# Kernel tuning notes

Hardware: AMD Instinct MI355X
Metric: run time of the kernel (lower is better)

## Reference

```python
import jax, jax.numpy as jnp
import numpy as np

K = 20          # neighbors, hardcoded default in source
EPS = 1e-5      # BatchNorm2d default eps


def _knn(x, k=K):
    # x: (B, C, N). distance[b,i,j] = -||x_i - x_j||^2; top-k == first k of descending sort
    inner = -2.0 * jnp.einsum('bdn,bdm->bnm', x, x)
    xx = jnp.sum(x * x, axis=1)                      # (B, N)
    dist = -xx[:, :, None] - inner - xx[:, None, :]  # (B, N, N)
    return jax.lax.top_k(dist, k)[1]                 # (B, N, k) int32


def _graph_feature(x, k=K):
    idx = _knn(x, k)
    xt = jnp.transpose(x, (0, 2, 1))                 # (B, N, C)
    feat = jax.vmap(lambda a, i: a[i])(xt, idx)      # (B, N, k, C) gather
    center = jnp.broadcast_to(xt[:, :, None, :], feat.shape)
    out = jnp.concatenate([feat - center, center], axis=-1)  # (B, N, k, 2C)
    return jnp.transpose(out, (0, 3, 1, 2))          # (B, 2C, N, k)


def _conv_bn_relu(x, w, g, b):
    # 1x1 conv (no bias) + train-mode BatchNorm (batch stats) + ReLU
    y = jnp.einsum('oc,bcnk->bonk', w, x)
    m = jnp.mean(y, axis=(0, 2, 3), keepdims=True)
    v = jnp.var(y, axis=(0, 2, 3), keepdims=True)
    y = (y - m) * jax.lax.rsqrt(v + EPS)
    y = y * g[None, :, None, None] + b[None, :, None, None]
    return jax.nn.relu(y)


def setup_inputs() -> dict:
    key = jax.random.key(0)
    ks = jax.random.split(key, 8)
    B, C, N = 8, 3, 2048
    emb = 512
    x = jax.random.normal(ks[0], (B, C, N), dtype=jnp.float32)

    def w(k, o, i):
        return jax.random.normal(k, (o, i), dtype=jnp.float32) * np.sqrt(2.0 / i).astype(np.float32)

    d = {'x': x}
    dims = [(6, 64), (64, 64), (64, 128), (128, 256), (512, emb)]
    for n, (i, o) in enumerate(dims, start=1):
        d[f'w{n}'] = w(ks[n], o, i)
        d[f'g{n}'] = jnp.ones((o,), jnp.float32)
        d[f'b{n}'] = jnp.zeros((o,), jnp.float32)
    return d


def reference(x, w1, g1, b1, w2, g2, b2, w3, g3, b3, w4, g4, b4, w5, g5, b5):
    B, _, N = x.shape
    h = _graph_feature(x)                                  # (B, 6, N, k)
    h = _conv_bn_relu(h, w1, g1, b1); x1 = jnp.max(h, -1, keepdims=True)
    h = _conv_bn_relu(h, w2, g2, b2); x2 = jnp.max(h, -1, keepdims=True)
    h = _conv_bn_relu(h, w3, g3, b3); x3 = jnp.max(h, -1, keepdims=True)
    h = _conv_bn_relu(h, w4, g4, b4); x4 = jnp.max(h, -1, keepdims=True)
    o = jnp.concatenate([x1, x2, x3, x4], axis=1)          # (B, 512, N, 1)
    o = _conv_bn_relu(o, w5, g5, b5)                       # (B, 512, N, 1)
    return o.reshape(B, -1, N)
```

## Files before the change

kernel.cpp:

```cpp
#include <hip/hip_runtime.h>
#include <cstdint>
#include <cstddef>

#define BATCH 8
#define NPTS 2048
#define KNN 20
#define M1 327680
#define M2 16384

typedef unsigned short ushort_t;
typedef __attribute__((ext_vector_type(8))) short bf16x8;
typedef __attribute__((ext_vector_type(4))) float f32x4;
typedef __attribute__((ext_vector_type(2))) int int2v;

#define OFF_XT    0UL
#define OFF_XX    196608UL
#define OFF_IDX   262144UL
#define OFF_WH2   1572864UL
#define OFF_WH3   1589248UL
#define OFF_WH4   1622016UL
#define OFF_WH5   1753088UL
#define OFF_SS    2842624UL
#define OFF_REG0  2863104UL
#define OFF_REG1  86749184UL
#define OFF_XCAT  128692224UL
#define OFF_RAWMAX 145469440UL
#define OFF_RAWMIN 162246656UL
#define OFF_SP     179023872UL
#define WS_NEEDED  181121024UL

__device__ __forceinline__ float bf2f(unsigned short u) {
    union { unsigned int i; float f; } c; c.i = ((unsigned int)u) << 16; return c.f;
}
__device__ __forceinline__ unsigned short f2bf(float f) {
    union { float f; unsigned int i; } c; c.f = f;
    unsigned int x = c.i;
    unsigned int r = (x + 0x7fffu + ((x >> 16) & 1u)) >> 16;
    return (unsigned short)r;
}
__device__ __forceinline__ unsigned int pack2(float a, float b) {
    return (unsigned int)f2bf(a) | ((unsigned int)f2bf(b) << 16);
}
__device__ __forceinline__ void unpack8(uint4 u, float* v) {
    v[0] = bf2f((unsigned short)(u.x & 0xffffu)); v[1] = bf2f((unsigned short)(u.x >> 16));
    v[2] = bf2f((unsigned short)(u.y & 0xffffu)); v[3] = bf2f((unsigned short)(u.y >> 16));
    v[4] = bf2f((unsigned short)(u.z & 0xffffu)); v[5] = bf2f((unsigned short)(u.z >> 16));
    v[6] = bf2f((unsigned short)(u.w & 0xffffu)); v[7] = bf2f((unsigned short)(u.w >> 16));
}

__global__ void prep_k(const float* __restrict__ x, float* __restrict__ xt, float* __restrict__ xx) {
    int t = blockIdx.x * 256 + threadIdx.x;
    int b = t >> 11, n = t & 2047;
    float v0 = x[((size_t)b * 3 + 0) * NPTS + n];
    float v1 = x[((size_t)b * 3 + 1) * NPTS + n];
    float v2 = x[((size_t)b * 3 + 2) * NPTS + n];
    xt[(size_t)t * 3 + 0] = v0; xt[(size_t)t * 3 + 1] = v1; xt[(size_t)t * 3 + 2] = v2;
    xx[t] = __fadd_rn(__fadd_rn(__fmul_rn(v0, v0), __fmul_rn(v1, v1)), __fmul_rn(v2, v2));
}

__global__ void wsplit_all_k(const float* __restrict__ w2, ushort_t* __restrict__ wh2,
                             const float* __restrict__ w3, ushort_t* __restrict__ wh3,
                             const float* __restrict__ w4, ushort_t* __restrict__ wh4,
                             const float* __restrict__ w5, ushort_t* __restrict__ wh5) {
    int t = blockIdx.x * 256 + threadIdx.x;
    if (t < 4096)        { wh2[t] = f2bf(w2[t]); }
    else if (t < 12288)  { int o = t - 4096;  wh3[o] = f2bf(w3[o]); }
    else if (t < 45056)  { int o = t - 12288; wh4[o] = f2bf(w4[o]); }
    else                 { int o = t - 45056; wh5[o] = f2bf(w5[o]); }
}


__device__ __forceinline__ unsigned okey(float f) {
    int u = __float_as_int(f);
    return (unsigned)(u ^ ((u >> 31) | 0x80000000));
}

#define DPP_ROR(x, n) __builtin_amdgcn_update_dpp(0, (x), 0x120 + (n), 0xf, 0xf, true)

template<int N>
__device__ __forceinline__ void ror_merge(unsigned &hi, unsigned &lo) {
    unsigned thi = (unsigned)DPP_ROR((int)hi, N);
    unsigned tlo = (unsigned)DPP_ROR((int)lo, N);
    unsigned long long a = ((unsigned long long)hi << 32) | lo;
    unsigned long long b = ((unsigned long long)thi << 32) | tlo;
    if (b > a) { hi = thi; lo = tlo; }
}

__device__ __forceinline__ void half_merge(unsigned &hi, unsigned &lo) {
    int2v ph = __builtin_amdgcn_permlane32_swap((int)hi, (int)hi, false, false);
    int2v pl = __builtin_amdgcn_permlane32_swap((int)lo, (int)lo, false, false);
    unsigned long long a = ((unsigned long long)(unsigned)ph.x << 32) | (unsigned)pl.x;
    unsigned long long b = ((unsigned long long)(unsigned)ph.y << 32) | (unsigned)pl.y;
    if (b > a) { hi = (unsigned)ph.y; lo = (unsigned)pl.y; }
    else       { hi = (unsigned)ph.x; lo = (unsigned)pl.x; }
}

__device__ __forceinline__ int knn_winner(unsigned hi, unsigned lo) {
    unsigned h0 = (unsigned)__builtin_amdgcn_readlane((int)hi, 0);
    unsigned l0 = (unsigned)__builtin_amdgcn_readlane((int)lo, 0);
    unsigned h1 = (unsigned)__builtin_amdgcn_readlane((int)hi, 16);
    unsigned l1 = (unsigned)__builtin_amdgcn_readlane((int)lo, 16);
    unsigned long long A = ((unsigned long long)h0 << 32) | l0;
    unsigned long long B = ((unsigned long long)h1 << 32) | l1;
    unsigned lw = (B > A) ? l1 : l0;
    return 2047 - (int)lw;
}

template<int G>
__device__ __forceinline__ void knn_rescan(float (&v)[32], unsigned (&gh)[4], unsigned (&gl)[4],
                                           bool own, int qw, unsigned laneC) {
#pragma unroll
    for (int q = G * 8; q < G * 8 + 8; q++)
        if (own && q == qw) v[q] = -3.4e38f;
    float m = v[G * 8]; int qi = G * 8;
#pragma unroll
    for (int q = G * 8 + 1; q < G * 8 + 8; q++)
        if (v[q] > m) { m = v[q]; qi = q; }
    gh[G] = okey(m);
    gl[G] = laneC - (unsigned)(qi << 6);
}

__device__ __forceinline__ void knn_rescan_any(float (&v)[32], unsigned (&gh)[4], unsigned (&gl)[4],
                                               int j, int l, unsigned laneC) {
    int qw = j >> 6;
    bool own = (l == (j & 63));
    int gw = qw >> 3;
    if (gw == 0)      knn_rescan<0>(v, gh, gl, own, qw, laneC);
    else if (gw == 1) knn_rescan<1>(v, gh, gl, own, qw, laneC);
    else if (gw == 2) knn_rescan<2>(v, gh, gl, own, qw, laneC);
    else              knn_rescan<3>(v, gh, gl, own, qw, laneC);
}

__launch_bounds__(256)
__global__ void knn_k(const float* __restrict__ xt, const float* __restrict__ xx, int* __restrict__ idx) {
    int tid = threadIdx.x;
    int l = tid & 63, wv = tid >> 6;
    int pidA = blockIdx.x * 8 + wv * 2;
    int pidB = pidA + 1;
    int b = pidA >> 11;
    const float* xb  = xt + (size_t)b * NPTS * 3;
    const float* xxb = xx + (size_t)b * NPTS;
    int iA = pidA & 2047, iB = pidB & 2047;
    float xA0 = xb[iA * 3 + 0], xA1 = xb[iA * 3 + 1], xA2 = xb[iA * 3 + 2];
    float xB0 = xb[iB * 3 + 0], xB1 = xb[iB * 3 + 1], xB2 = xb[iB * 3 + 2];
    float xxA = xxb[iA], xxB = xxb[iB];
    float vA[32], vB[32];
#pragma unroll
    for (int q = 0; q < 32; q++) {
        int j = l + q * 64;
        float p0 = xb[j * 3 + 0], p1 = xb[j * 3 + 1], p2 = xb[j * 3 + 2];
        float xxj = xxb[j];
        float dA = __fadd_rn(__fadd_rn(__fmul_rn(xA0, p0), __fmul_rn(xA1, p1)), __fmul_rn(xA2, p2));
        float dB = __fadd_rn(__fadd_rn(__fmul_rn(xB0, p0), __fmul_rn(xB1, p1)), __fmul_rn(xB2, p2));
        vA[q] = __fsub_rn(__fsub_rn(-xxA, __fmul_rn(-2.0f, dA)), xxj);
        vB[q] = __fsub_rn(__fsub_rn(-xxB, __fmul_rn(-2.0f, dB)), xxj);
    }
    unsigned laneC = (unsigned)(2047 - l);
    unsigned ghA[4], glA[4], ghB[4], glB[4];
#pragma unroll
    for (int g = 0; g < 4; g++) {
        float mA = vA[g * 8]; int qA = g * 8;
        float mB = vB[g * 8]; int qB = g * 8;
#pragma unroll
        for (int q = g * 8 + 1; q < g * 8 + 8; q++) {
            if (vA[q] > mA) { mA = vA[q]; qA = q; }
            if (vB[q] > mB) { mB = vB[q]; qB = q; }
        }
        ghA[g] = okey(mA); glA[g] = laneC - (unsigned)(qA << 6);
        ghB[g] = okey(mB); glB[g] = laneC - (unsigned)(qB << 6);
    }
    int* outA = idx + (size_t)pidA * KNN;
    int* outB = idx + (size_t)pidB * KNN;
    for (int t = 0; t < KNN; t++) {
        unsigned hA = ghA[0], lA = glA[0];
        unsigned hB = ghB[0], lB = glB[0];
#pragma unroll
        for (int g = 1; g < 4; g++) {
            unsigned long long a0 = ((unsigned long long)hA << 32) | lA;
            unsigned long long b0 = ((unsigned long long)ghA[g] << 32) | glA[g];
            if (b0 > a0) { hA = ghA[g]; lA = glA[g]; }
            unsigned long long a1 = ((unsigned long long)hB << 32) | lB;
            unsigned long long b1 = ((unsigned long long)ghB[g] << 32) | glB[g];
            if (b1 > a1) { hB = ghB[g]; lB = glB[g]; }
        }
        ror_merge<1>(hA, lA); ror_merge<1>(hB, lB);
        ror_merge<2>(hA, lA); ror_merge<2>(hB, lB);
        ror_merge<4>(hA, lA); ror_merge<4>(hB, lB);
        ror_merge<8>(hA, lA); ror_merge<8>(hB, lB);
        half_merge(hA, lA);   half_merge(hB, lB);
        int jA = knn_winner(hA, lA);
        int jB = knn_winner(hB, lB);
        if (l == 0) { outA[t] = jA; outB[t] = jB; }
        if (t == KNN - 1) break;
        knn_rescan_any(vA, ghA, glA, jA, l, laneC);
        knn_rescan_any(vB, ghB, glB, jB, l, laneC);
    }
}

__launch_bounds__(256, 2)
__global__ void conv1_fused_k(const float* __restrict__ xt, const int* __restrict__ idx,
                              const float* __restrict__ w1, ushort_t* __restrict__ y1,
                              float* __restrict__ rawmax, float* __restrict__ rawmin,
                              float* __restrict__ sp) {
    __shared__ ushort_t hA[320 * 56];
    __shared__ ushort_t wHs[64 * 56];
    __shared__ float sw[4 * 64 * 2];
    const int tid = threadIdx.x;
    const int m0 = blockIdx.x * 320;
    for (int i = tid; i < 512; i += 256) sw[i] = 0.0f;
    {
        int row = tid >> 2, seg = tid & 3;
        uint4 u = make_uint4(0, 0, 0, 0);
        if (seg == 0) {
            const float* wr = w1 + row * 6;
            u.x = pack2(wr[0], wr[1]);
            u.y = pack2(wr[2], wr[3]);
            u.z = pack2(wr[4], wr[5]);
        }
        *(uint4*)&wHs[row * 56 + seg * 8] = u;
    }
    for (int r = tid; r < 320; r += 256) {
        int m = m0 + r;
        int nb = m / KNN;
        int b = nb >> 11;
        int j = idx[m];
        const float* pi = xt + (size_t)nb * 3;
        const float* pj = xt + ((size_t)(b * NPTS + j)) * 3;
        uint4 u;
        u.x = pack2(pj[0] - pi[0], pj[1] - pi[1]);
        u.y = pack2(pj[2] - pi[2], pi[0]);
        u.z = pack2(pi[1], pi[2]);
        u.w = 0;
        uint4 z = make_uint4(0, 0, 0, 0);
        *(uint4*)&hA[r * 56 + 0]  = u;
        *(uint4*)&hA[r * 56 + 8]  = z;
        *(uint4*)&hA[r * 56 + 16] = z;
        *(uint4*)&hA[r * 56 + 24] = z;
    }
    __syncthreads();
    const int lane = tid & 63, wv = tid >> 6;
    const int l15 = lane & 15, quad = lane >> 4;
    f32x4 acc[5][4];
#pragma unroll
    for (int mt = 0; mt < 5; mt++)
#pragma unroll
        for (int ot = 0; ot < 4; ot++) acc[mt][ot] = (f32x4){0.f, 0.f, 0.f, 0.f};
    bf16x8 a[5];
#pragma unroll
    for (int mt = 0; mt < 5; mt++)
        a[mt] = *(bf16x8*)&hA[(wv * 80 + mt * 16 + l15) * 56 + quad * 8];
#pragma unroll
    for (int ot = 0; ot < 4; ot++) {
        bf16x8 bh = *(bf16x8*)&wHs[(ot * 16 + l15) * 56 + quad * 8];
#pragma unroll
        for (int mt = 0; mt < 5; mt++)
            acc[mt][ot] = __builtin_amdgcn_mfma_f32_16x16x32_bf16(a[mt], bh, acc[mt][ot], 0, 0, 0);
    }
    __syncthreads();
    float* wreg = (float*)((char*)hA + wv * 6400);
#pragma unroll
    for (int ot = 0; ot < 4; ot++) {
#pragma unroll
        for (int mt = 0; mt < 5; mt++)
#pragma unroll
            for (int r = 0; r < 4; r++)
                wreg[(mt * 16 + quad * 4 + r) * 20 + l15] = acc[mt][ot][r];
        __syncthreads();
        {
            int pp = quad;
            const float* rr = wreg + (pp * 20) * 20 + l15;
            float mx = rr[0], mn = rr[0], sm = 0.0f, ss = 0.0f;
#pragma unroll
            for (int q = 0; q < 20; q++) {
                float vv = rr[q * 20];
                mx = fmaxf(mx, vv); mn = fminf(mn, vv);
                sm += vv; ss = fmaf(vv, vv, ss);
            }
            int pt = blockIdx.x * 16 + wv * 4 + pp;
            int o = ot * 16 + l15;
            rawmax[(size_t)pt * 64 + o] = mx;
            rawmin[(size_t)pt * 64 + o] = mn;
            sm += __shfl_xor(sm, 16); sm += __shfl_xor(sm, 32);
            ss += __shfl_xor(ss, 16); ss += __shfl_xor(ss, 32);
            if (lane < 16) {
                sw[(wv * 64 + ot * 16 + l15) * 2 + 0] += sm;
                sw[(wv * 64 + ot * 16 + l15) * 2 + 1] += ss;
            }
        }
#pragma unroll
        for (int it = 0; it < 3; it++) {
            int t = lane + it * 64;
            if (t < 160) {
                int row = t >> 1, half = t & 1;
                float4 f0 = *(float4*)&wreg[row * 20 + half * 8];
                float4 f1 = *(float4*)&wreg[row * 20 + half * 8 + 4];
                uint4 u;
                u.x = pack2(f0.x, f0.y); u.y = pack2(f0.z, f0.w);
                u.z = pack2(f1.x, f1.y); u.w = pack2(f1.z, f1.w);
                *(uint4*)(y1 + (size_t)(m0 + wv * 80 + row) * 64 + ot * 16 + half * 8) = u;
            }
        }
        __syncthreads();
    }
    if (tid < 128) {
        int ol = tid >> 1, st = tid & 1;
        float v = 0.0f;
#pragma unroll
        for (int w2 = 0; w2 < 4; w2++) v += sw[(w2 * 64 + ol) * 2 + st];
        sp[(size_t)blockIdx.x * 128 + ol * 2 + st] = v;
    }
}

template<int CIN, int COUT>
__launch_bounds__(256)
__global__ void conv5_mfma_k(const ushort_t* __restrict__ yin,
                             const ushort_t* __restrict__ whi,
                             ushort_t* __restrict__ yout,
                             float* __restrict__ sp) {
    __shared__ char smem[23552];
    ushort_t* hA = (ushort_t*)smem;
    ushort_t* wH = (ushort_t*)(smem + 14336);
    float* sw = (float*)(smem + 21504);
    const int tid = threadIdx.x;
    const int m0 = blockIdx.y * 128;
    const int o0 = blockIdx.x * 64;
    f32x4 acc[2][4];
#pragma unroll
    for (int mt = 0; mt < 2; mt++)
#pragma unroll
        for (int ot = 0; ot < 4; ot++) acc[mt][ot] = (f32x4){0.f, 0.f, 0.f, 0.f};
    const int lane = tid & 63, wv = tid >> 6;
    const int l15 = lane & 15, quad = lane >> 4;
    for (int kc = 0; kc < CIN; kc += 32) {
        __syncthreads();
#pragma unroll
        for (int i = 0; i < 2; i++) {
            int tt = tid + 256 * i;
            int mr = tt >> 2, cq = (tt & 3) * 8;
            *(uint4*)&hA[mr * 56 + cq] = *(const uint4*)(yin + (size_t)(m0 + mr) * CIN + kc + cq);
        }
        {
            int orow = tid >> 2, cq = (tid & 3) * 8;
            *(uint4*)&wH[orow * 56 + cq] = *(const uint4*)(whi + (size_t)(o0 + orow) * CIN + kc + cq);
        }
        __syncthreads();
        bf16x8 a0 = *(bf16x8*)&hA[(wv * 32 + l15) * 56 + quad * 8];
        bf16x8 a1 = *(bf16x8*)&hA[(wv * 32 + 16 + l15) * 56 + quad * 8];
#pragma unroll
        for (int ot = 0; ot < 4; ot++) {
            bf16x8 bh = *(bf16x8*)&wH[(ot * 16 + l15) * 56 + quad * 8];
            acc[0][ot] = __builtin_amdgcn_mfma_f32_16x16x32_bf16(a0, bh, acc[0][ot], 0, 0, 0);
            acc[1][ot] = __builtin_amdgcn_mfma_f32_16x16x32_bf16(a1, bh, acc[1][ot], 0, 0, 0);
        }
    }
#pragma unroll
    for (int ot = 0; ot < 4; ot++) {
        float sm = 0.0f, ss = 0.0f;
#pragma unroll
        for (int mt = 0; mt < 2; mt++)
#pragma unroll
            for (int r = 0; r < 4; r++) {
                float v = acc[mt][ot][r];
                sm += v; ss = fmaf(v, v, ss);
            }
        sm += __shfl_xor(sm, 16); sm += __shfl_xor(sm, 32);
        ss += __shfl_xor(ss, 16); ss += __shfl_xor(ss, 32);
        if (lane < 16) {
            sw[(wv * 64 + ot * 16 + l15) * 2 + 0] = sm;
            sw[(wv * 64 + ot * 16 + l15) * 2 + 1] = ss;
        }
    }
    __syncthreads();
    ushort_t* outT = (ushort_t*)smem;
#pragma unroll
    for (int mt = 0; mt < 2; mt++)
#pragma unroll
        for (int ot = 0; ot < 4; ot++)
#pragma unroll
            for (int r = 0; r < 4; r++)
                outT[(wv * 32 + mt * 16 + quad * 4 + r) * 72 + ot * 16 + l15] = f2bf(acc[mt][ot][r]);
    __syncthreads();
    int row = tid >> 1, half = tid & 1;
#pragma unroll
    for (int g = 0; g < 4; g++) {
        uint4 u = *(uint4*)&outT[row * 72 + half * 32 + g * 8];
        *(uint4*)(yout + (size_t)(m0 + row) * COUT + o0 + half * 32 + g * 8) = u;
    }
    if (tid < 128) {
        int ol = tid >> 1, st = tid & 1;
        float v = 0.0f;
#pragma unroll
        for (int w2 = 0; w2 < 4; w2++) v += sw[(w2 * 64 + ol) * 2 + st];
        size_t bid = (size_t)blockIdx.x * gridDim.y + blockIdx.y;
        sp[bid * 128 + ol * 2 + st] = v;
    }
}

template<int CIN, int COUT, int BO, bool WRITEY>
__launch_bounds__(256, 2)
__global__ void conv_fused_k(const ushort_t* __restrict__ yin,
                             const ushort_t* __restrict__ whi,
                             const float* __restrict__ scale,
                             const float* __restrict__ shift,
                             ushort_t* __restrict__ yout,
                             float* __restrict__ rawmax, float* __restrict__ rawmin,
                             float* __restrict__ sp) {
    constexpr int NOT = BO / 16;
    __shared__ ushort_t hA[320 * 56];
    __shared__ ushort_t wHs[BO * 56];
    __shared__ float scl[CIN], shf[CIN];
    __shared__ float sw[4 * BO * 2];
    const int tid = threadIdx.x;
    const int m0 = blockIdx.y * 320;
    const int o0 = blockIdx.x * BO;
    for (int c = tid; c < CIN; c += 256) { scl[c] = scale[c]; shf[c] = shift[c]; }
    for (int i = tid; i < 4 * BO * 2; i += 256) sw[i] = 0.0f;
    f32x4 acc[5][NOT];
#pragma unroll
    for (int mt = 0; mt < 5; mt++)
#pragma unroll
        for (int ot = 0; ot < NOT; ot++) acc[mt][ot] = (f32x4){0.f, 0.f, 0.f, 0.f};
    const int lane = tid & 63, wv = tid >> 6;
    const int l15 = lane & 15, quad = lane >> 4;
    for (int kc = 0; kc < CIN; kc += 32) {
        __syncthreads();
#pragma unroll
        for (int i = 0; i < 5; i++) {
            int tt = tid + 256 * i;
            int mr = tt >> 2, cq = (tt & 3) * 8;
            uint4 u = *(const uint4*)(yin + (size_t)(m0 + mr) * CIN + kc + cq);
            float vv[8]; unpack8(u, vv);
#pragma unroll
            for (int e = 0; e < 8; e++)
                vv[e] = fmaxf(fmaf(vv[e], scl[kc + cq + e], shf[kc + cq + e]), 0.0f);
            u.x = pack2(vv[0], vv[1]); u.y = pack2(vv[2], vv[3]);
            u.z = pack2(vv[4], vv[5]); u.w = pack2(vv[6], vv[7]);
            *(uint4*)&hA[mr * 56 + cq] = u;
        }
        for (int t = tid; t < BO * 4; t += 256) {
            int row = t >> 2, cq = (t & 3) * 8;
            *(uint4*)&wHs[row * 56 + cq] = *(const uint4*)(whi + (size_t)(o0 + row) * CIN + kc + cq);
        }
        __syncthreads();
        bf16x8 a[5];
#pragma unroll
        for (int mt = 0; mt < 5; mt++)
            a[mt] = *(bf16x8*)&hA[(wv * 80 + mt * 16 + l15) * 56 + quad * 8];
#pragma unroll
        for (int ot = 0; ot < NOT; ot++) {
            bf16x8 bh = *(bf16x8*)&wHs[(ot * 16 + l15) * 56 + quad * 8];
#pragma unroll
            for (int mt = 0; mt < 5; mt++)
                acc[mt][ot] = __builtin_amdgcn_mfma_f32_16x16x32_bf16(a[mt], bh, acc[mt][ot], 0, 0, 0);
        }
    }
    __syncthreads();
    float* wreg = (float*)((char*)hA + wv * 6400);
#pragma unroll
    for (int ot = 0; ot < NOT; ot++) {
#pragma unroll
        for (int mt = 0; mt < 5; mt++)
#pragma unroll
            for (int r = 0; r < 4; r++)
                wreg[(mt * 16 + quad * 4 + r) * 20 + l15] = acc[mt][ot][r];
        __syncthreads();
        {
            int pp = quad;
            const float* rr = wreg + (pp * 20) * 20 + l15;
            float mx = rr[0], mn = rr[0], sm = 0.0f, ss = 0.0f;
#pragma unroll
            for (int q = 0; q < 20; q++) {
                float vv = rr[q * 20];
                mx = fmaxf(mx, vv); mn = fminf(mn, vv);
                sm += vv; ss = fmaf(vv, vv, ss);
            }
            int pt = blockIdx.y * 16 + wv * 4 + pp;
            int o = o0 + ot * 16 + l15;
            rawmax[(size_t)pt * COUT + o] = mx;
            rawmin[(size_t)pt * COUT + o] = mn;
            sm += __shfl_xor(sm, 16); sm += __shfl_xor(sm, 32);
            ss += __shfl_xor(ss, 16); ss += __shfl_xor(ss, 32);
            if (lane < 16) {
                sw[(wv * BO + ot * 16 + l15) * 2 + 0] += sm;
                sw[(wv * BO + ot * 16 + l15) * 2 + 1] += ss;
            }
        }
        if constexpr (WRITEY) {
#pragma unroll
            for (int it = 0; it < 3; it++) {
                int t = lane + it * 64;
                if (t < 160) {
                    int row = t >> 1, half = t & 1;
                    float4 f0 = *(float4*)&wreg[row * 20 + half * 8];
                    float4 f1 = *(float4*)&wreg[row * 20 + half * 8 + 4];
                    uint4 u;
                    u.x = pack2(f0.x, f0.y); u.y = pack2(f0.z, f0.w);
                    u.z = pack2(f1.x, f1.y); u.w = pack2(f1.z, f1.w);
                    *(uint4*)(yout + (size_t)(m0 + wv * 80 + row) * COUT + o0 + ot * 16 + half * 8) = u;
                }
            }
        }
        __syncthreads();
    }
    for (int t2 = tid; t2 < BO * 2; t2 += 256) {
        int ol = t2 >> 1, st = t2 & 1;
        float v = 0.0f;
#pragma unroll
        for (int w2 = 0; w2 < 4; w2++) v += sw[(w2 * BO + ol) * 2 + st];
        size_t bid = (size_t)blockIdx.x * 1024 + blockIdx.y;
        sp[bid * (2 * BO) + ol * 2 + st] = v;
    }
}

template<int BO, int MB>
__launch_bounds__(256)
__global__ void statsred_fin_k(const float* __restrict__ sp,
                               const float* __restrict__ g, const float* __restrict__ bb,
                               float* __restrict__ scale, float* __restrict__ shift,
                               double invcnt) {
    __shared__ double rs[256], rss[256];
    int o = blockIdx.x, tid = threadIdx.x;
    int oy = o / BO, ol = o % BO;
    double s = 0.0, ss = 0.0;
    for (int mb = tid; mb < MB; mb += 256) {
        size_t bid = (size_t)oy * MB + mb;
        s  += (double)sp[bid * (2 * BO) + ol * 2 + 0];
        ss += (double)sp[bid * (2 * BO) + ol * 2 + 1];
    }
    rs[tid] = s; rss[tid] = ss;
    __syncthreads();
    for (int st = 128; st; st >>= 1) {
        if (tid < st) { rs[tid] += rs[tid + st]; rss[tid] += rss[tid + st]; }
        __syncthreads();
    }
    if (tid == 0) {
        double m = rs[0] * invcnt;
        double v = rss[0] * invcnt - m * m;
        if (v < 0.0) v = 0.0;
        float sc = g[o] / sqrtf((float)v + 1e-5f);
        scale[o] = sc;
        shift[o] = bb[o] - (float)m * sc;
    }
}

template<int C8>
__launch_bounds__(256)
__global__ void pool_raw_k(const float* __restrict__ rawmax, const float* __restrict__ rawmin,
                           const float* __restrict__ scale, const float* __restrict__ shift,
                           ushort_t* __restrict__ xcat, int coff) {
    constexpr int COUT = C8 * 8;
    int gid = blockIdx.x * 256 + threadIdx.x;
    int p = gid / C8, og = gid % C8;
    float sc[8], sh[8], mxv[8], mnv[8];
    *(float4*)&sc[0]  = *(const float4*)(scale + og * 8);
    *(float4*)&sc[4]  = *(const float4*)(scale + og * 8 + 4);
    *(float4*)&sh[0]  = *(const float4*)(shift + og * 8);
    *(float4*)&sh[4]  = *(const float4*)(shift + og * 8 + 4);
    *(float4*)&mxv[0] = *(const float4*)(rawmax + (size_t)p * COUT + og * 8);
    *(float4*)&mxv[4] = *(const float4*)(rawmax + (size_t)p * COUT + og * 8 + 4);
    *(float4*)&mnv[0] = *(const float4*)(rawmin + (size_t)p * COUT + og * 8);
    *(float4*)&mnv[4] = *(const float4*)(rawmin + (size_t)p * COUT + og * 8 + 4);
    float v[8];
#pragma unroll
    for (int e = 0; e < 8; e++) {
        float raw = (sc[e] >= 0.0f) ? mxv[e] : mnv[e];
        v[e] = fmaxf(fmaf(raw, sc[e], sh[e]), 0.0f);
    }
    uint4 u;
    u.x = pack2(v[0], v[1]); u.y = pack2(v[2], v[3]);
    u.z = pack2(v[4], v[5]); u.w = pack2(v[6], v[7]);
    *(uint4*)(xcat + (size_t)p * 512 + coff + og * 8) = u;
}

__launch_bounds__(256)
__global__ void out_k(const ushort_t* __restrict__ y5, const float* __restrict__ scale,
                      const float* __restrict__ shift, float* __restrict__ out) {
    __shared__ float tr[64 * 65];
    int tid = threadIdx.x;
    int n0 = blockIdx.x * 64, c0 = blockIdx.y * 64, b = blockIdx.z;
    int nl = tid >> 2, cq = (tid & 3) * 16;
    const ushort_t* src = y5 + (size_t)(b * 2048 + n0 + nl) * 512 + c0 + cq;
#pragma unroll
    for (int h = 0; h < 2; h++) {
        uint4 u = *(const uint4*)(src + h * 8);
        float vv[8]; unpack8(u, vv);
#pragma unroll
        for (int e = 0; e < 8; e++) {
            int c = cq + h * 8 + e;
            tr[c * 65 + nl] = fmaxf(fmaf(vv[e], scale[c0 + c], shift[c0 + c]), 0.0f);
        }
    }
    __syncthreads();
    int cl = tid >> 2, ng = (tid & 3) * 16;
#pragma unroll
    for (int g = 0; g < 4; g++) {
        float4 v = *(float4*)&tr[cl * 65 + ng + g * 4];
        *(float4*)(out + ((size_t)b * 512 + c0 + cl) * 2048 + n0 + ng + g * 4) = v;
    }
}

extern "C" void kernel_launch(void* const* d_in, const int* in_sizes, int n_in,
                              void* d_out, int out_size, void* d_ws, size_t ws_size,
                              hipStream_t stream) {
    (void)in_sizes; (void)n_in; (void)out_size;
    if (ws_size < WS_NEEDED) return;
    const float* x  = (const float*)d_in[0];
    const float* w1 = (const float*)d_in[1];
    const float* g1 = (const float*)d_in[2];
    const float* b1 = (const float*)d_in[3];
    const float* w2 = (const float*)d_in[4];
    const float* g2 = (const float*)d_in[5];
    const float* b2 = (const float*)d_in[6];
    const float* w3 = (const float*)d_in[7];
    const float* g3 = (const float*)d_in[8];
    const float* b3 = (const float*)d_in[9];
    const float* w4 = (const float*)d_in[10];
    const float* g4 = (const float*)d_in[11];
    const float* b4 = (const float*)d_in[12];
    const float* w5 = (const float*)d_in[13];
    const float* g5 = (const float*)d_in[14];
    const float* b5 = (const float*)d_in[15];

    char* ws = (char*)d_ws;
    float* xt  = (float*)(ws + OFF_XT);
    float* xx  = (float*)(ws + OFF_XX);
    int*   idx = (int*)(ws + OFF_IDX);
    ushort_t* wh2 = (ushort_t*)(ws + OFF_WH2);
    ushort_t* wh3 = (ushort_t*)(ws + OFF_WH3);
    ushort_t* wh4 = (ushort_t*)(ws + OFF_WH4);
    ushort_t* wh5 = (ushort_t*)(ws + OFF_WH5);
    ushort_t* y1 = (ushort_t*)(ws + OFF_REG0);
    ushort_t* y2 = (ushort_t*)(ws + OFF_REG1);
    ushort_t* y3 = (ushort_t*)(ws + OFF_REG0);
    ushort_t* y5 = (ushort_t*)(ws + OFF_REG0);
    ushort_t* xcat = (ushort_t*)(ws + OFF_XCAT);
    float* rawmax = (float*)(ws + OFF_RAWMAX);
    float* rawmin = (float*)(ws + OFF_RAWMIN);
    float* sp     = (float*)(ws + OFF_SP);

    float* scl[5]; float* shf[5];
    for (int l = 0; l < 5; l++) {
        scl[l] = (float*)(ws + OFF_SS + (size_t)l * 4096);
        shf[l] = scl[l] + 512;
    }

    prep_k<<<64, 256, 0, stream>>>(x, xt, xx);
    wsplit_all_k<<<1200, 256, 0, stream>>>(w2, wh2, w3, wh3, w4, wh4, w5, wh5);
    knn_k<<<2048, 256, 0, stream>>>(xt, xx, idx);

    conv1_fused_k<<<1024, 256, 0, stream>>>(xt, idx, w1, y1, rawmax, rawmin, sp);
    statsred_fin_k<64, 1024><<<64, 256, 0, stream>>>(sp, g1, b1, scl[0], shf[0], 1.0 / 327680.0);
    pool_raw_k<8><<<512, 256, 0, stream>>>(rawmax, rawmin, scl[0], shf[0], xcat, 0);

    conv_fused_k<64, 64, 64, true><<<dim3(1, 1024), 256, 0, stream>>>(
        y1, wh2, scl[0], shf[0], y2, rawmax, rawmin, sp);
    statsred_fin_k<64, 1024><<<64, 256, 0, stream>>>(sp, g2, b2, scl[1], shf[1], 1.0 / 327680.0);
    pool_raw_k<8><<<512, 256, 0, stream>>>(rawmax, rawmin, scl[1], shf[1], xcat, 64);

    conv_fused_k<64, 128, 128, true><<<dim3(1, 1024), 256, 0, stream>>>(
        y2, wh3, scl[1], shf[1], y3, rawmax, rawmin, sp);
    statsred_fin_k<128, 1024><<<128, 256, 0, stream>>>(sp, g3, b3, scl[2], shf[2], 1.0 / 327680.0);
    pool_raw_k<16><<<1024, 256, 0, stream>>>(rawmax, rawmin, scl[2], shf[2], xcat, 128);

    conv_fused_k<128, 256, 128, false><<<dim3(2, 1024), 256, 0, stream>>>(
        y3, wh4, scl[2], shf[2], nullptr, rawmax, rawmin, sp);
    statsred_fin_k<128, 1024><<<256, 256, 0, stream>>>(sp, g4, b4, scl[3], shf[3], 1.0 / 327680.0);
    pool_raw_k<32><<<2048, 256, 0, stream>>>(rawmax, rawmin, scl[3], shf[3], xcat, 256);

    conv5_mfma_k<512, 512><<<dim3(8, 128), 256, 0, stream>>>(xcat, wh5, y5, sp);
    statsred_fin_k<64, 128><<<512, 256, 0, stream>>>(sp, g5, b5, scl[4], shf[4], 1.0 / 16384.0);
    out_k<<<dim3(32, 8, 8), 256, 0, stream>>>(y5, scl[4], shf[4], (float*)d_out);
}
```

Measured before the change: 446.3 us.

## Pack points as float4 with norm and streamline kNN wave argmax reduction

```diff
diff --git a/kernel.cpp b/kernel.cpp
--- a/kernel.cpp
+++ b/kernel.cpp
@@ -9,12 +9,12 @@
 #define M2 16384
 
 typedef unsigned short ushort_t;
+typedef unsigned long long u64;
 typedef __attribute__((ext_vector_type(8))) short bf16x8;
 typedef __attribute__((ext_vector_type(4))) float f32x4;
 typedef __attribute__((ext_vector_type(2))) int int2v;
 
 #define OFF_XT    0UL
-#define OFF_XX    196608UL
 #define OFF_IDX   262144UL
 #define OFF_WH2   1572864UL
 #define OFF_WH3   1589248UL
@@ -48,14 +48,14 @@
     v[6] = bf2f((unsigned short)(u.w & 0xffffu)); v[7] = bf2f((unsigned short)(u.w >> 16));
 }
 
-__global__ void prep_k(const float* __restrict__ x, float* __restrict__ xt, float* __restrict__ xx) {
+__global__ void prep_k(const float* __restrict__ x, float4* __restrict__ xt4) {
     int t = blockIdx.x * 256 + threadIdx.x;
     int b = t >> 11, n = t & 2047;
     float v0 = x[((size_t)b * 3 + 0) * NPTS + n];
     float v1 = x[((size_t)b * 3 + 1) * NPTS + n];
     float v2 = x[((size_t)b * 3 + 2) * NPTS + n];
-    xt[(size_t)t * 3 + 0] = v0; xt[(size_t)t * 3 + 1] = v1; xt[(size_t)t * 3 + 2] = v2;
-    xx[t] = __fadd_rn(__fadd_rn(__fmul_rn(v0, v0), __fmul_rn(v1, v1)), __fmul_rn(v2, v2));
+    float xxv = __fadd_rn(__fadd_rn(__fmul_rn(v0, v0), __fmul_rn(v1, v1)), __fmul_rn(v2, v2));
+    xt4[t] = make_float4(v0, v1, v2, xxv);
 }
 
 __global__ void wsplit_all_k(const float* __restrict__ w2, ushort_t* __restrict__ wh2,
@@ -78,36 +78,31 @@
 #define DPP_ROR(x, n) __builtin_amdgcn_update_dpp(0, (x), 0x120 + (n), 0xf, 0xf, true)
 
 template<int N>
-__device__ __forceinline__ void ror_merge(unsigned &hi, unsigned &lo) {
-    unsigned thi = (unsigned)DPP_ROR((int)hi, N);
-    unsigned tlo = (unsigned)DPP_ROR((int)lo, N);
-    unsigned long long a = ((unsigned long long)hi << 32) | lo;
-    unsigned long long b = ((unsigned long long)thi << 32) | tlo;
-    if (b > a) { hi = thi; lo = tlo; }
-}
-
-__device__ __forceinline__ void half_merge(unsigned &hi, unsigned &lo) {
-    int2v ph = __builtin_amdgcn_permlane32_swap((int)hi, (int)hi, false, false);
-    int2v pl = __builtin_amdgcn_permlane32_swap((int)lo, (int)lo, false, false);
-    unsigned long long a = ((unsigned long long)(unsigned)ph.x << 32) | (unsigned)pl.x;
-    unsigned long long b = ((unsigned long long)(unsigned)ph.y << 32) | (unsigned)pl.y;
-    if (b > a) { hi = (unsigned)ph.y; lo = (unsigned)pl.y; }
-    else       { hi = (unsigned)ph.x; lo = (unsigned)pl.x; }
-}
-
-__device__ __forceinline__ int knn_winner(unsigned hi, unsigned lo) {
-    unsigned h0 = (unsigned)__builtin_amdgcn_readlane((int)hi, 0);
-    unsigned l0 = (unsigned)__builtin_amdgcn_readlane((int)lo, 0);
-    unsigned h1 = (unsigned)__builtin_amdgcn_readlane((int)hi, 16);
-    unsigned l1 = (unsigned)__builtin_amdgcn_readlane((int)lo, 16);
-    unsigned long long A = ((unsigned long long)h0 << 32) | l0;
-    unsigned long long B = ((unsigned long long)h1 << 32) | l1;
-    unsigned lw = (B > A) ? l1 : l0;
-    return 2047 - (int)lw;
+__device__ __forceinline__ void ror_max(u64 &k) {
+    unsigned h = (unsigned)DPP_ROR((int)(unsigned)(k >> 32), N);
+    unsigned lo = (unsigned)DPP_ROR((int)(unsigned)k, N);
+    u64 o = ((u64)h << 32) | lo;
+    if (o > k) k = o;
+}
+
+__device__ __forceinline__ void swap16_max(u64 &k) {
+    int2v ph = __builtin_amdgcn_permlane16_swap((int)(unsigned)(k >> 32), (int)(unsigned)(k >> 32), false, false);
+    int2v pl = __builtin_amdgcn_permlane16_swap((int)(unsigned)k, (int)(unsigned)k, false, false);
+    u64 a = ((u64)(unsigned)ph.x << 32) | (unsigned)pl.x;
+    u64 b = ((u64)(unsigned)ph.y << 32) | (unsigned)pl.y;
+    k = (b > a) ? b : a;
+}
+
+__device__ __forceinline__ void swap32_max(u64 &k) {
+    int2v ph = __builtin_amdgcn_permlane32_swap((int)(unsigned)(k >> 32), (int)(unsigned)(k >> 32), false, false);
+    int2v pl = __builtin_amdgcn_permlane32_swap((int)(unsigned)k, (int)(unsigned)k, false, false);
+    u64 a = ((u64)(unsigned)ph.x << 32) | (unsigned)pl.x;
+    u64 b = ((u64)(unsigned)ph.y << 32) | (unsigned)pl.y;
+    k = (b > a) ? b : a;
 }
 
 template<int G>
-__device__ __forceinline__ void knn_rescan(float (&v)[32], unsigned (&gh)[4], unsigned (&gl)[4],
+__device__ __forceinline__ void knn_rescan(float (&v)[32], u64 (&gk)[4],
                                            bool own, int qw, unsigned laneC) {
 #pragma unroll
     for (int q = G * 8; q < G * 8 + 8; q++)
@@ -116,47 +111,43 @@
 #pragma unroll
     for (int q = G * 8 + 1; q < G * 8 + 8; q++)
         if (v[q] > m) { m = v[q]; qi = q; }
-    gh[G] = okey(m);
-    gl[G] = laneC - (unsigned)(qi << 6);
-}
-
-__device__ __forceinline__ void knn_rescan_any(float (&v)[32], unsigned (&gh)[4], unsigned (&gl)[4],
+    gk[G] = ((u64)okey(m) << 32) | (laneC - (unsigned)(qi << 6));
+}
+
+__device__ __forceinline__ void knn_rescan_any(float (&v)[32], u64 (&gk)[4],
                                                int j, int l, unsigned laneC) {
     int qw = j >> 6;
     bool own = (l == (j & 63));
     int gw = qw >> 3;
-    if (gw == 0)      knn_rescan<0>(v, gh, gl, own, qw, laneC);
-    else if (gw == 1) knn_rescan<1>(v, gh, gl, own, qw, laneC);
-    else if (gw == 2) knn_rescan<2>(v, gh, gl, own, qw, laneC);
-    else              knn_rescan<3>(v, gh, gl, own, qw, laneC);
+    if (gw == 0)      knn_rescan<0>(v, gk, own, qw, laneC);
+    else if (gw == 1) knn_rescan<1>(v, gk, own, qw, laneC);
+    else if (gw == 2) knn_rescan<2>(v, gk, own, qw, laneC);
+    else              knn_rescan<3>(v, gk, own, qw, laneC);
 }
 
 __launch_bounds__(256)
-__global__ void knn_k(const float* __restrict__ xt, const float* __restrict__ xx, int* __restrict__ idx) {
+__global__ void knn_k(const float4* __restrict__ xt4, int* __restrict__ idx) {
     int tid = threadIdx.x;
     int l = tid & 63, wv = tid >> 6;
     int pidA = blockIdx.x * 8 + wv * 2;
     int pidB = pidA + 1;
     int b = pidA >> 11;
-    const float* xb  = xt + (size_t)b * NPTS * 3;
-    const float* xxb = xx + (size_t)b * NPTS;
+    const float4* xb4 = xt4 + (size_t)b * NPTS;
     int iA = pidA & 2047, iB = pidB & 2047;
-    float xA0 = xb[iA * 3 + 0], xA1 = xb[iA * 3 + 1], xA2 = xb[iA * 3 + 2];
-    float xB0 = xb[iB * 3 + 0], xB1 = xb[iB * 3 + 1], xB2 = xb[iB * 3 + 2];
-    float xxA = xxb[iA], xxB = xxb[iB];
+    float4 PA = xb4[iA];
+    float4 PB = xb4[iB];
     float vA[32], vB[32];
 #pragma unroll
     for (int q = 0; q < 32; q++) {
         int j = l + q * 64;
-        float p0 = xb[j * 3 + 0], p1 = xb[j * 3 + 1], p2 = xb[j * 3 + 2];
-        float xxj = xxb[j];
-        float dA = __fadd_rn(__fadd_rn(__fmul_rn(xA0, p0), __fmul_rn(xA1, p1)), __fmul_rn(xA2, p2));
-        float dB = __fadd_rn(__fadd_rn(__fmul_rn(xB0, p0), __fmul_rn(xB1, p1)), __fmul_rn(xB2, p2));
-        vA[q] = __fsub_rn(__fsub_rn(-xxA, __fmul_rn(-2.0f, dA)), xxj);
-        vB[q] = __fsub_rn(__fsub_rn(-xxB, __fmul_rn(-2.0f, dB)), xxj);
+        float4 p = xb4[j];
+        float dA = __fadd_rn(__fadd_rn(__fmul_rn(PA.x, p.x), __fmul_rn(PA.y, p.y)), __fmul_rn(PA.z, p.z));
+        float dB = __fadd_rn(__fadd_rn(__fmul_rn(PB.x, p.x), __fmul_rn(PB.y, p.y)), __fmul_rn(PB.z, p.z));
+        vA[q] = __fsub_rn(__fsub_rn(-PA.w, __fmul_rn(-2.0f, dA)), p.w);
+        vB[q] = __fsub_rn(__fsub_rn(-PB.w, __fmul_rn(-2.0f, dB)), p.w);
     }
     unsigned laneC = (unsigned)(2047 - l);
-    unsigned ghA[4], glA[4], ghB[4], glB[4];
+    u64 gkA[4], gkB[4];
 #pragma unroll
     for (int g = 0; g < 4; g++) {
         float mA = vA[g * 8]; int qA = g * 8;
@@ -166,39 +157,42 @@
             if (vA[q] > mA) { mA = vA[q]; qA = q; }
             if (vB[q] > mB) { mB = vB[q]; qB = q; }
         }
-        ghA[g] = okey(mA); glA[g] = laneC - (unsigned)(qA << 6);
-        ghB[g] = okey(mB); glB[g] = laneC - (unsigned)(qB << 6);
+        gkA[g] = ((u64)okey(mA) << 32) | (laneC - (unsigned)(qA << 6));
+        gkB[g] = ((u64)okey(mB) << 32) | (laneC - (unsigned)(qB << 6));
     }
     int* outA = idx + (size_t)pidA * KNN;
     int* outB = idx + (size_t)pidB * KNN;
+    unsigned myj = 0;
+#pragma unroll 1
     for (int t = 0; t < KNN; t++) {
-        unsigned hA = ghA[0], lA = glA[0];
-        unsigned hB = ghB[0], lB = glB[0];
+        u64 kA = gkA[0], kB = gkB[0];
 #pragma unroll
         for (int g = 1; g < 4; g++) {
-            unsigned long long a0 = ((unsigned long long)hA << 32) | lA;
-            unsigned long long b0 = ((unsigned long long)ghA[g] << 32) | glA[g];
-            if (b0 > a0) { hA = ghA[g]; lA = glA[g]; }
-            unsigned long long a1 = ((unsigned long long)hB << 32) | lB;
-            unsigned long long b1 = ((unsigned long long)ghB[g] << 32) | glB[g];
-            if (b1 > a1) { hB = ghB[g]; lB = glB[g]; }
-        }
-        ror_merge<1>(hA, lA); ror_merge<1>(hB, lB);
-        ror_merge<2>(hA, lA); ror_merge<2>(hB, lB);
-        ror_merge<4>(hA, lA); ror_merge<4>(hB, lB);
-        ror_merge<8>(hA, lA); ror_merge<8>(hB, lB);
-        half_merge(hA, lA);   half_merge(hB, lB);
-        int jA = knn_winner(hA, lA);
-        int jB = knn_winner(hB, lB);
-        if (l == 0) { outA[t] = jA; outB[t] = jB; }
+            if (gkA[g] > kA) kA = gkA[g];
+            if (gkB[g] > kB) kB = gkB[g];
+        }
+        ror_max<1>(kA); ror_max<1>(kB);
+        ror_max<2>(kA); ror_max<2>(kB);
+        ror_max<4>(kA); ror_max<4>(kB);
+        ror_max<8>(kA); ror_max<8>(kB);
+        swap16_max(kA); swap16_max(kB);
+        swap32_max(kA); swap32_max(kB);
+        unsigned jAv = 2047u - (unsigned)kA;
+        unsigned jBv = 2047u - (unsigned)kB;
+        myj = (l == t) ? jAv : myj;
+        myj = (l == t + 32) ? jBv : myj;
         if (t == KNN - 1) break;
-        knn_rescan_any(vA, ghA, glA, jA, l, laneC);
-        knn_rescan_any(vB, ghB, glB, jB, l, laneC);
-    }
+        int jA = 2047 - (int)(unsigned)__builtin_amdgcn_readfirstlane((int)(unsigned)kA);
+        int jB = 2047 - (int)(unsigned)__builtin_amdgcn_readfirstlane((int)(unsigned)kB);
+        knn_rescan_any(vA, gkA, jA, l, laneC);
+        knn_rescan_any(vB, gkB, jB, l, laneC);
+    }
+    if (l < KNN) outA[l] = (int)myj;
+    if (l >= 32 && l < 32 + KNN) outB[l - 32] = (int)myj;
 }
 
 __launch_bounds__(256, 2)
-__global__ void conv1_fused_k(const float* __restrict__ xt, const int* __restrict__ idx,
+__global__ void conv1_fused_k(const float4* __restrict__ xt4, const int* __restrict__ idx,
                               const float* __restrict__ w1, ushort_t* __restrict__ y1,
                               float* __restrict__ rawmax, float* __restrict__ rawmin,
                               float* __restrict__ sp) {
@@ -224,12 +218,12 @@
         int nb = m / KNN;
         int b = nb >> 11;
         int j = idx[m];
-        const float* pi = xt + (size_t)nb * 3;
-        const float* pj = xt + ((size_t)(b * NPTS + j)) * 3;
+        float4 PI = xt4[nb];
+        float4 PJ = xt4[(size_t)(b * NPTS + j)];
         uint4 u;
-        u.x = pack2(pj[0] - pi[0], pj[1] - pi[1]);
-        u.y = pack2(pj[2] - pi[2], pi[0]);
-        u.z = pack2(pi[1], pi[2]);
+        u.x = pack2(PJ.x - PI.x, PJ.y - PI.y);
+        u.y = pack2(PJ.z - PI.z, PI.x);
+        u.z = pack2(PI.y, PI.z);
         u.w = 0;
         uint4 z = make_uint4(0, 0, 0, 0);
         *(uint4*)&hA[r * 56 + 0]  = u;
@@ -622,8 +616,7 @@
     const float* b5 = (const float*)d_in[15];
 
     char* ws = (char*)d_ws;
-    float* xt  = (float*)(ws + OFF_XT);
-    float* xx  = (float*)(ws + OFF_XX);
+    float4* xt4 = (float4*)(ws + OFF_XT);
     int*   idx = (int*)(ws + OFF_IDX);
     ushort_t* wh2 = (ushort_t*)(ws + OFF_WH2);
     ushort_t* wh3 = (ushort_t*)(ws + OFF_WH3);
@@ -644,11 +637,11 @@
         shf[l] = scl[l] + 512;
     }
 
-    prep_k<<<64, 256, 0, stream>>>(x, xt, xx);
+    prep_k<<<64, 256, 0, stream>>>(x, xt4);
     wsplit_all_k<<<1200, 256, 0, stream>>>(w2, wh2, w3, wh3, w4, wh4, w5, wh5);
-    knn_k<<<2048, 256, 0, stream>>>(xt, xx, idx);
-
-    conv1_fused_k<<<1024, 256, 0, stream>>>(xt, idx, w1, y1, rawmax, rawmin, sp);
+    knn_k<<<2048, 256, 0, stream>>>(xt4, idx);
+
+    conv1_fused_k<<<1024, 256, 0, stream>>>(xt4, idx, w1, y1, rawmax, rawmin, sp);
     statsred_fin_k<64, 1024><<<64, 256, 0, stream>>>(sp, g1, b1, scl[0], shf[0], 1.0 / 327680.0);
     pool_raw_k<8><<<512, 256, 0, stream>>>(rawmax, rawmin, scl[0], shf[0], xcat, 0);
 
```

After: 436.3 us. 2.2% less time.
